# Performance work log

Measured on AMD Instinct MI355X. Metric: run time of the kernel, lower is better.

Reference implementation:

```python
import jax, jax.numpy as jnp
import numpy as np

B, L, D_IN = 32, 200, 64
H = 64          # hidden_size
A = 36          # attention_size
NEG_SLOPE = 0.01  # torch LeakyReLU default


def setup_inputs() -> dict:
    key = jax.random.key(0)
    ks = jax.random.split(key, 7)
    s_ln = 1.0 / np.sqrt(D_IN)
    s_w1 = 1.0 / np.sqrt(3 * H)
    s_w2 = 1.0 / np.sqrt(A)
    return {
        "x": jax.random.normal(ks[0], (B, L, D_IN), dtype=jnp.float32),
        "ln_w": jax.random.uniform(ks[1], (D_IN, H), minval=-s_ln, maxval=s_ln, dtype=jnp.float32),
        "ln_b": jax.random.uniform(ks[2], (H,), minval=-s_ln, maxval=s_ln, dtype=jnp.float32),
        "w1": jax.random.uniform(ks[3], (3 * H, A), minval=-s_w1, maxval=s_w1, dtype=jnp.float32),
        "b1": jax.random.uniform(ks[4], (A,), minval=-s_w1, maxval=s_w1, dtype=jnp.float32),
        "w2": jax.random.uniform(ks[5], (A,), minval=-s_w2, maxval=s_w2, dtype=jnp.float32),
        "b2": jax.random.uniform(ks[6], (), minval=-s_w2, maxval=s_w2, dtype=jnp.float32),
    }


def reference(x, ln_w, ln_b, w1, b1, w2, b2):
    # x: [B, L, D_in] -> h: [B, L, H]
    h = jnp.einsum("bld,dh->blh", x, ln_w) + ln_b
    Ld = h.shape[1]
    Hd = h.shape[-1]
    # The torch code concatenates (x1, x2, x1*x2) where x1[b,i,j]=h[b,j],
    # x2[b,i,j]=h[b,i]. Split w1 accordingly instead of materializing the
    # [B,L,L,3H] concat tensor.
    w1a, w1b, w1c = w1[:Hd], w1[Hd:2 * Hd], w1[2 * Hd:]
    a = jnp.einsum("bjh,ha->bja", h, w1a)          # x1 contribution (depends on j)
    c = jnp.einsum("bih,ha->bia", h, w1b)          # x2 contribution (depends on i)
    cross = jnp.einsum("bih,bjh,ha->bija", h, h, w1c)  # (x1*x2) contribution
    pre = a[:, None, :, :] + c[:, :, None, :] + cross + b1   # [B,L,L,A]
    act = jax.nn.leaky_relu(pre, negative_slope=NEG_SLOPE)
    score = jnp.einsum("bija,a->bij", act, w2) + b2          # [B,L,L]
    mask = jnp.tril(jnp.ones((Ld, Ld), dtype=score.dtype))   # causal (incl. diag)
    score = score * mask
    return jnp.einsum("bij,bjh->bih", score, h)               # [B,L,H]
```

## Files before the change

kernel.cpp:

```cpp
#include <hip/hip_runtime.h>

#define B 32
#define L 200
#define DIN 64
#define H 64
#define A 36

typedef __attribute__((ext_vector_type(8))) short short8;
typedef __attribute__((ext_vector_type(4))) float floatx4;
typedef __attribute__((ext_vector_type(8))) float floatx8;

static __device__ __forceinline__ short f2bf(float f) {
    union { float f; unsigned u; } v; v.f = f;
    unsigned r = (v.u + 0x7FFF + ((v.u >> 16) & 1)) >> 16;
    return (short)r;
}

__global__ __launch_bounds__(256) void prep_kernel(
    const float* __restrict__ x, const float* __restrict__ ln_w,
    const float* __restrict__ ln_b, const float* __restrict__ w1,
    float* __restrict__ h_out, float* __restrict__ cc_out, short* __restrict__ hb16_out,
    float* __restrict__ w1a_r, float* __restrict__ w1c_r)
{
    int wave = threadIdx.x >> 6;
    int lane = threadIdx.x & 63;
    int bl = __builtin_amdgcn_readfirstlane(blockIdx.x * 4 + wave);
    const float* xr = x + (size_t)bl * DIN;
    float p0 = ln_b[lane], p1 = 0.f;
    #pragma unroll
    for (int d = 0; d < DIN; d += 2) {
        p0 = fmaf(xr[d],     ln_w[d * H + lane],       p0);
        p1 = fmaf(xr[d + 1], ln_w[(d + 1) * H + lane], p1);
    }
    float acc = p0 + p1;
    __shared__ float hrow[4][H];
    hrow[wave][lane] = acc;
    h_out[(size_t)bl * H + lane] = acc;
    int j = bl % L;
    hb16_out[(size_t)bl * H + (lane ^ ((j & 7) << 3))] = f2bf(acc);
    if (lane < A) {
        float s0 = 0.f, s1 = 0.f;
        #pragma unroll
        for (int hh = 0; hh < H; hh += 2) {
            s0 = fmaf(hrow[wave][hh],     w1[(H + hh) * A + lane],     s0);
            s1 = fmaf(hrow[wave][hh + 1], w1[(H + hh + 1) * A + lane], s1);
        }
        cc_out[(size_t)bl * A + lane] = s0 + s1;
    }
    if (blockIdx.x == 0) {
        for (int idx = threadIdx.x; idx < 2 * 3 * 64 * 8; idx += 256) {
            int e = idx & 7, ln = (idx >> 3) & 63, sn = idx >> 9;
            int s = sn / 3, n = sn - 3 * s;
            int k = s * 32 + (ln >> 4) * 8 + e;
            int c = n * 16 + (ln & 15);
            w1a_r[idx] = (c < A) ? w1[k * A + c] : 0.f;
            w1c_r[idx] = (c < A) ? w1[(2 * H + k) * A + c] : 0.f;
        }
    }
}

__global__ __launch_bounds__(256) void score_kernel(
    const float* __restrict__ h, const short* __restrict__ hb16,
    const float* __restrict__ cc, const float* __restrict__ w1a_r,
    const float* __restrict__ w1c_r, const float* __restrict__ b1,
    const float* __restrict__ w2, const float* __restrict__ b2,
    float* __restrict__ out)
{
    int blk = blockIdx.x;
    int b  = blk / 50;
    int g  = 49 - (blk - b * 50);
    int wave = threadIdx.x >> 6;
    int lane = threadIdx.x & 63;
    int i = __builtin_amdgcn_readfirstlane(4 * g + wave);
    int l15 = lane & 15, l4 = lane >> 4;

    __shared__ __align__(16) short tile[208 * 64];

    const short* hb16b = hb16 + (size_t)b * L * H;
    const float* h_b   = h + (size_t)b * L * H;

    int maxrow = 4 * g + 3;
    int nch = (((maxrow | 15) + 1) + 7) >> 3;
    for (int c = wave; c < nch; c += 4) {
        int j = c * 8 + (lane >> 3); if (j > L - 1) j = L - 1;
        const short* src = hb16b + (size_t)j * H + (lane & 7) * 8;
        __builtin_amdgcn_global_load_lds(
            (const __attribute__((address_space(1))) void*)src,
            (__attribute__((address_space(3))) void*)&tile[c * 512],
            16, 0, 0);
    }

    const float* hi = h_b + (size_t)i * H;
    float b2v = b2[0];
    float ccl = (lane < A) ? (cc[((size_t)b * L + i) * A + lane] + b1[lane]) : 0.f;
    float w2l = (lane < A) ? w2[lane] : 0.f;
    float w2v[3][4], cbv[3][4];
    #pragma unroll
    for (int n = 0; n < 3; ++n) {
        #pragma unroll
        for (int r = 0; r < 4; ++r) {
            int a = n * 16 + l4 * 4 + r;
            cbv[n][r] = __shfl(ccl, a, 64);
            w2v[n][r] = __shfl(w2l, a, 64);
        }
    }
    short8 afrag[2][3];
    #pragma unroll
    for (int s = 0; s < 2; ++s) {
        float hik[8];
        #pragma unroll
        for (int e = 0; e < 8; ++e) hik[e] = hi[s * 32 + l4 * 8 + e];
        #pragma unroll
        for (int n = 0; n < 3; ++n) {
            floatx8 wa = *(const floatx8*)&w1a_r[(((s * 3 + n) * 64) + lane) * 8];
            floatx8 wc = *(const floatx8*)&w1c_r[(((s * 3 + n) * 64) + lane) * 8];
            #pragma unroll
            for (int e = 0; e < 8; ++e)
                afrag[s][n][e] = f2bf(fmaf(hik[e], wc[e], wa[e]));
        }
    }
    __syncthreads();

    float oacc[4] = {0.f, 0.f, 0.f, 0.f};
    int mmax = (i >> 4) + 1;
    int sw = (l15 & 7) << 3;

    const short* brow0 = tile + l15 * 64;
    short8 bfc0 = *(const short8*)(brow0 + ((l4 * 8) ^ sw));
    short8 bfc1 = *(const short8*)(brow0 + ((32 + l4 * 8) ^ sw));

    for (int m = 0; m < mmax; ++m) {
        short8 bfn0, bfn1;
        if (m + 1 < mmax) {
            const short* brown = tile + ((m + 1) * 16 + l15) * 64;
            bfn0 = *(const short8*)(brown + ((l4 * 8) ^ sw));
            bfn1 = *(const short8*)(brown + ((32 + l4 * 8) ^ sw));
        }
        int row = m * 16 + l15;
        floatx4 c0 = {cbv[0][0], cbv[0][1], cbv[0][2], cbv[0][3]};
        floatx4 c1 = {cbv[1][0], cbv[1][1], cbv[1][2], cbv[1][3]};
        floatx4 c2 = {cbv[2][0], cbv[2][1], cbv[2][2], cbv[2][3]};
        c0 = __builtin_amdgcn_mfma_f32_16x16x32_bf16(afrag[0][0], bfc0, c0, 0, 0, 0);
        c1 = __builtin_amdgcn_mfma_f32_16x16x32_bf16(afrag[0][1], bfc0, c1, 0, 0, 0);
        c2 = __builtin_amdgcn_mfma_f32_16x16x32_bf16(afrag[0][2], bfc0, c2, 0, 0, 0);
        c0 = __builtin_amdgcn_mfma_f32_16x16x32_bf16(afrag[1][0], bfc1, c0, 0, 0, 0);
        c1 = __builtin_amdgcn_mfma_f32_16x16x32_bf16(afrag[1][1], bfc1, c1, 0, 0, 0);
        c2 = __builtin_amdgcn_mfma_f32_16x16x32_bf16(afrag[1][2], bfc1, c2, 0, 0, 0);
        float sp0 = 0.f, sp1 = 0.f, sp2 = 0.f;
        #pragma unroll
        for (int r = 0; r < 4; ++r) {
            sp0 = fmaf(fmaxf(c0[r], 0.01f * c0[r]), w2v[0][r], sp0);
            sp1 = fmaf(fmaxf(c1[r], 0.01f * c1[r]), w2v[1][r], sp1);
            sp2 = fmaf(fmaxf(c2[r], 0.01f * c2[r]), w2v[2][r], sp2);
        }
        float sp = (sp0 + sp1) + sp2;
        sp += __shfl_xor(sp, 16, 64);
        sp += __shfl_xor(sp, 32, 64);
        float sc = (row <= i) ? sp + b2v : 0.f;

        const float* hjb = h_b + (size_t)(m * 16) * H + lane;
        #pragma unroll
        for (int rb = 0; rb < 4; ++rb) {
            #pragma unroll
            for (int q = 0; q < 4; ++q) {
                int jq = rb * 4 + q;
                float sq = __int_as_float(
                    __builtin_amdgcn_readlane(__float_as_int(sc), jq));
                float hv = hjb[jq * H];
                oacc[rb] = fmaf(sq, hv, oacc[rb]);
            }
        }
        bfc0 = bfn0;
        bfc1 = bfn1;
    }

    out[((size_t)b * L + i) * H + lane] = (oacc[0] + oacc[1]) + (oacc[2] + oacc[3]);
}

extern "C" void kernel_launch(void* const* d_in, const int* in_sizes, int n_in,
                              void* d_out, int out_size, void* d_ws, size_t ws_size,
                              hipStream_t stream) {
    const float* x    = (const float*)d_in[0];
    const float* ln_w = (const float*)d_in[1];
    const float* ln_b = (const float*)d_in[2];
    const float* w1   = (const float*)d_in[3];
    const float* b1   = (const float*)d_in[4];
    const float* w2   = (const float*)d_in[5];
    const float* b2   = (const float*)d_in[6];
    float* out = (float*)d_out;

    float* h_ws   = (float*)d_ws;
    float* cc_ws  = h_ws + (size_t)B * L * H;
    short* hb16_ws = (short*)(cc_ws + (size_t)B * L * A);
    float* w1a_r  = (float*)(hb16_ws + (size_t)B * L * H);
    float* w1c_r  = w1a_r + 3072;

    prep_kernel<<<(B * L) / 4, 256, 0, stream>>>(x, ln_w, ln_b, w1, h_ws, cc_ws,
                                                 hb16_ws, w1a_r, w1c_r);
    score_kernel<<<B * 50, 256, 0, stream>>>(h_ws, hb16_ws, cc_ws, w1a_r, w1c_r,
                                             b1, w2, b2, out);
}
```

Before: 38.28 us.

## Move x2 projection into score kernel and process two j-tiles per iteration

Drops the per-row cc projection (h·w1b) from the prep kernel and recomputes it inside the score kernel from the register-resident h_i values, using a repacked w1b and cross-lane shuffles. This removes the cc workspace write/read and prep's shared-memory pass. The score loop is unrolled to handle two 16-row j tiles per iteration with interleaved MFMAs, replacing the prior register double-buffering of B fragments, and launch_bounds is removed from score_kernel. The cost is more register pressure and extra per-block FMAs in the score kernel.

```diff
diff --git a/kernel.cpp b/kernel.cpp
--- a/kernel.cpp
+++ b/kernel.cpp
@@ -19,8 +19,8 @@
 __global__ __launch_bounds__(256) void prep_kernel(
     const float* __restrict__ x, const float* __restrict__ ln_w,
     const float* __restrict__ ln_b, const float* __restrict__ w1,
-    float* __restrict__ h_out, float* __restrict__ cc_out, short* __restrict__ hb16_out,
-    float* __restrict__ w1a_r, float* __restrict__ w1c_r)
+    float* __restrict__ h_out, short* __restrict__ hb16_out,
+    float* __restrict__ w1a_r, float* __restrict__ w1b_r, float* __restrict__ w1c_r)
 {
     int wave = threadIdx.x >> 6;
     int lane = threadIdx.x & 63;
@@ -33,35 +33,26 @@
         p1 = fmaf(xr[d + 1], ln_w[(d + 1) * H + lane], p1);
     }
     float acc = p0 + p1;
-    __shared__ float hrow[4][H];
-    hrow[wave][lane] = acc;
     h_out[(size_t)bl * H + lane] = acc;
     int j = bl % L;
     hb16_out[(size_t)bl * H + (lane ^ ((j & 7) << 3))] = f2bf(acc);
-    if (lane < A) {
-        float s0 = 0.f, s1 = 0.f;
-        #pragma unroll
-        for (int hh = 0; hh < H; hh += 2) {
-            s0 = fmaf(hrow[wave][hh],     w1[(H + hh) * A + lane],     s0);
-            s1 = fmaf(hrow[wave][hh + 1], w1[(H + hh + 1) * A + lane], s1);
-        }
-        cc_out[(size_t)bl * A + lane] = s0 + s1;
-    }
     if (blockIdx.x == 0) {
         for (int idx = threadIdx.x; idx < 2 * 3 * 64 * 8; idx += 256) {
             int e = idx & 7, ln = (idx >> 3) & 63, sn = idx >> 9;
             int s = sn / 3, n = sn - 3 * s;
             int k = s * 32 + (ln >> 4) * 8 + e;
             int c = n * 16 + (ln & 15);
-            w1a_r[idx] = (c < A) ? w1[k * A + c] : 0.f;
-            w1c_r[idx] = (c < A) ? w1[(2 * H + k) * A + c] : 0.f;
-        }
-    }
-}
-
-__global__ __launch_bounds__(256) void score_kernel(
+            bool cv = c < A;
+            w1a_r[idx] = cv ? w1[k * A + c] : 0.f;
+            w1b_r[idx] = cv ? w1[(H + k) * A + c] : 0.f;
+            w1c_r[idx] = cv ? w1[(2 * H + k) * A + c] : 0.f;
+        }
+    }
+}
+
+__global__ void score_kernel(
     const float* __restrict__ h, const short* __restrict__ hb16,
-    const float* __restrict__ cc, const float* __restrict__ w1a_r,
+    const float* __restrict__ w1a_r, const float* __restrict__ w1b_r,
     const float* __restrict__ w1c_r, const float* __restrict__ b1,
     const float* __restrict__ w2, const float* __restrict__ b2,
     float* __restrict__ out)
@@ -92,31 +83,44 @@
 
     const float* hi = h_b + (size_t)i * H;
     float b2v = b2[0];
-    float ccl = (lane < A) ? (cc[((size_t)b * L + i) * A + lane] + b1[lane]) : 0.f;
-    float w2l = (lane < A) ? w2[lane] : 0.f;
+    float hik[2][8];
+    #pragma unroll
+    for (int s = 0; s < 2; ++s) {
+        floatx8 hv = *(const floatx8*)(hi + s * 32 + l4 * 8);
+        #pragma unroll
+        for (int e = 0; e < 8; ++e) hik[s][e] = hv[e];
+    }
+    float ccn[3];
+    short8 afrag[2][3];
+    #pragma unroll
+    for (int n = 0; n < 3; ++n) ccn[n] = 0.f;
+    #pragma unroll
+    for (int s = 0; s < 2; ++s) {
+        #pragma unroll
+        for (int n = 0; n < 3; ++n) {
+            int base = (((s * 3 + n) * 64) + lane) * 8;
+            floatx8 wa = *(const floatx8*)&w1a_r[base];
+            floatx8 wb = *(const floatx8*)&w1b_r[base];
+            floatx8 wc = *(const floatx8*)&w1c_r[base];
+            #pragma unroll
+            for (int e = 0; e < 8; ++e) {
+                afrag[s][n][e] = f2bf(fmaf(hik[s][e], wc[e], wa[e]));
+                ccn[n] = fmaf(hik[s][e], wb[e], ccn[n]);
+            }
+        }
+    }
     float w2v[3][4], cbv[3][4];
     #pragma unroll
     for (int n = 0; n < 3; ++n) {
+        ccn[n] += __shfl_xor(ccn[n], 16, 64);
+        ccn[n] += __shfl_xor(ccn[n], 32, 64);
+        int c = n * 16 + l15;
+        float cb = (c < A) ? (ccn[n] + b1[c]) : 0.f;
         #pragma unroll
         for (int r = 0; r < 4; ++r) {
             int a = n * 16 + l4 * 4 + r;
-            cbv[n][r] = __shfl(ccl, a, 64);
-            w2v[n][r] = __shfl(w2l, a, 64);
-        }
-    }
-    short8 afrag[2][3];
-    #pragma unroll
-    for (int s = 0; s < 2; ++s) {
-        float hik[8];
-        #pragma unroll
-        for (int e = 0; e < 8; ++e) hik[e] = hi[s * 32 + l4 * 8 + e];
-        #pragma unroll
-        for (int n = 0; n < 3; ++n) {
-            floatx8 wa = *(const floatx8*)&w1a_r[(((s * 3 + n) * 64) + lane) * 8];
-            floatx8 wc = *(const floatx8*)&w1c_r[(((s * 3 + n) * 64) + lane) * 8];
-            #pragma unroll
-            for (int e = 0; e < 8; ++e)
-                afrag[s][n][e] = f2bf(fmaf(hik[e], wc[e], wa[e]));
+            cbv[n][r] = __shfl(cb, l4 * 4 + r, 16);
+            w2v[n][r] = (a < A) ? w2[a] : 0.f;
         }
     }
     __syncthreads();
@@ -124,40 +128,92 @@
     float oacc[4] = {0.f, 0.f, 0.f, 0.f};
     int mmax = (i >> 4) + 1;
     int sw = (l15 & 7) << 3;
-
-    const short* brow0 = tile + l15 * 64;
-    short8 bfc0 = *(const short8*)(brow0 + ((l4 * 8) ^ sw));
-    short8 bfc1 = *(const short8*)(brow0 + ((32 + l4 * 8) ^ sw));
-
-    for (int m = 0; m < mmax; ++m) {
-        short8 bfn0, bfn1;
-        if (m + 1 < mmax) {
-            const short* brown = tile + ((m + 1) * 16 + l15) * 64;
-            bfn0 = *(const short8*)(brown + ((l4 * 8) ^ sw));
-            bfn1 = *(const short8*)(brown + ((32 + l4 * 8) ^ sw));
-        }
+    int m = 0;
+
+    for (; m + 1 < mmax; m += 2) {
+        int rowA = m * 16 + l15, rowB = rowA + 16;
+        const short* browA = tile + rowA * 64;
+        const short* browB = tile + rowB * 64;
+        short8 a0 = *(const short8*)(browA + ((l4 * 8) ^ sw));
+        short8 a1 = *(const short8*)(browA + ((32 + l4 * 8) ^ sw));
+        short8 bb0 = *(const short8*)(browB + ((l4 * 8) ^ sw));
+        short8 bb1 = *(const short8*)(browB + ((32 + l4 * 8) ^ sw));
+        floatx4 cA0 = {cbv[0][0], cbv[0][1], cbv[0][2], cbv[0][3]};
+        floatx4 cA1 = {cbv[1][0], cbv[1][1], cbv[1][2], cbv[1][3]};
+        floatx4 cA2 = {cbv[2][0], cbv[2][1], cbv[2][2], cbv[2][3]};
+        floatx4 cB0 = cA0, cB1 = cA1, cB2 = cA2;
+        cA0 = __builtin_amdgcn_mfma_f32_16x16x32_bf16(afrag[0][0], a0, cA0, 0, 0, 0);
+        cB0 = __builtin_amdgcn_mfma_f32_16x16x32_bf16(afrag[0][0], bb0, cB0, 0, 0, 0);
+        cA1 = __builtin_amdgcn_mfma_f32_16x16x32_bf16(afrag[0][1], a0, cA1, 0, 0, 0);
+        cB1 = __builtin_amdgcn_mfma_f32_16x16x32_bf16(afrag[0][1], bb0, cB1, 0, 0, 0);
+        cA2 = __builtin_amdgcn_mfma_f32_16x16x32_bf16(afrag[0][2], a0, cA2, 0, 0, 0);
+        cB2 = __builtin_amdgcn_mfma_f32_16x16x32_bf16(afrag[0][2], bb0, cB2, 0, 0, 0);
+        cA0 = __builtin_amdgcn_mfma_f32_16x16x32_bf16(afrag[1][0], a1, cA0, 0, 0, 0);
+        cB0 = __builtin_amdgcn_mfma_f32_16x16x32_bf16(afrag[1][0], bb1, cB0, 0, 0, 0);
+        cA1 = __builtin_amdgcn_mfma_f32_16x16x32_bf16(afrag[1][1], a1, cA1, 0, 0, 0);
+        cB1 = __builtin_amdgcn_mfma_f32_16x16x32_bf16(afrag[1][1], bb1, cB1, 0, 0, 0);
+        cA2 = __builtin_amdgcn_mfma_f32_16x16x32_bf16(afrag[1][2], a1, cA2, 0, 0, 0);
+        cB2 = __builtin_amdgcn_mfma_f32_16x16x32_bf16(afrag[1][2], bb1, cB2, 0, 0, 0);
+        float sA0 = 0.f, sA1 = 0.f, sA2 = 0.f, sB0 = 0.f, sB1 = 0.f, sB2 = 0.f;
+        #pragma unroll
+        for (int r = 0; r < 4; ++r) {
+            sA0 = fmaf(fmaxf(cA0[r], 0.01f * cA0[r]), w2v[0][r], sA0);
+            sB0 = fmaf(fmaxf(cB0[r], 0.01f * cB0[r]), w2v[0][r], sB0);
+            sA1 = fmaf(fmaxf(cA1[r], 0.01f * cA1[r]), w2v[1][r], sA1);
+            sB1 = fmaf(fmaxf(cB1[r], 0.01f * cB1[r]), w2v[1][r], sB1);
+            sA2 = fmaf(fmaxf(cA2[r], 0.01f * cA2[r]), w2v[2][r], sA2);
+            sB2 = fmaf(fmaxf(cB2[r], 0.01f * cB2[r]), w2v[2][r], sB2);
+        }
+        float spA = (sA0 + sA1) + sA2;
+        float spB = (sB0 + sB1) + sB2;
+        spA += __shfl_xor(spA, 16, 64);
+        spB += __shfl_xor(spB, 16, 64);
+        spA += __shfl_xor(spA, 32, 64);
+        spB += __shfl_xor(spB, 32, 64);
+        float scA = (rowA <= i) ? spA + b2v : 0.f;
+        float scB = (rowB <= i) ? spB + b2v : 0.f;
+
+        const float* hjA = h_b + (size_t)(m * 16) * H + lane;
+        const float* hjB = hjA + 16 * H;
+        #pragma unroll
+        for (int rb = 0; rb < 4; ++rb) {
+            #pragma unroll
+            for (int q = 0; q < 4; ++q) {
+                int jq = rb * 4 + q;
+                float sqA = __int_as_float(
+                    __builtin_amdgcn_readlane(__float_as_int(scA), jq));
+                float sqB = __int_as_float(
+                    __builtin_amdgcn_readlane(__float_as_int(scB), jq));
+                oacc[rb] = fmaf(sqA, hjA[jq * H], oacc[rb]);
+                oacc[rb] = fmaf(sqB, hjB[jq * H], oacc[rb]);
+            }
+        }
+    }
+    if (m < mmax) {
         int row = m * 16 + l15;
+        const short* brow = tile + row * 64;
+        short8 a0 = *(const short8*)(brow + ((l4 * 8) ^ sw));
+        short8 a1 = *(const short8*)(brow + ((32 + l4 * 8) ^ sw));
         floatx4 c0 = {cbv[0][0], cbv[0][1], cbv[0][2], cbv[0][3]};
         floatx4 c1 = {cbv[1][0], cbv[1][1], cbv[1][2], cbv[1][3]};
         floatx4 c2 = {cbv[2][0], cbv[2][1], cbv[2][2], cbv[2][3]};
-        c0 = __builtin_amdgcn_mfma_f32_16x16x32_bf16(afrag[0][0], bfc0, c0, 0, 0, 0);
-        c1 = __builtin_amdgcn_mfma_f32_16x16x32_bf16(afrag[0][1], bfc0, c1, 0, 0, 0);
-        c2 = __builtin_amdgcn_mfma_f32_16x16x32_bf16(afrag[0][2], bfc0, c2, 0, 0, 0);
-        c0 = __builtin_amdgcn_mfma_f32_16x16x32_bf16(afrag[1][0], bfc1, c0, 0, 0, 0);
-        c1 = __builtin_amdgcn_mfma_f32_16x16x32_bf16(afrag[1][1], bfc1, c1, 0, 0, 0);
-        c2 = __builtin_amdgcn_mfma_f32_16x16x32_bf16(afrag[1][2], bfc1, c2, 0, 0, 0);
-        float sp0 = 0.f, sp1 = 0.f, sp2 = 0.f;
+        c0 = __builtin_amdgcn_mfma_f32_16x16x32_bf16(afrag[0][0], a0, c0, 0, 0, 0);
+        c1 = __builtin_amdgcn_mfma_f32_16x16x32_bf16(afrag[0][1], a0, c1, 0, 0, 0);
+        c2 = __builtin_amdgcn_mfma_f32_16x16x32_bf16(afrag[0][2], a0, c2, 0, 0, 0);
+        c0 = __builtin_amdgcn_mfma_f32_16x16x32_bf16(afrag[1][0], a1, c0, 0, 0, 0);
+        c1 = __builtin_amdgcn_mfma_f32_16x16x32_bf16(afrag[1][1], a1, c1, 0, 0, 0);
+        c2 = __builtin_amdgcn_mfma_f32_16x16x32_bf16(afrag[1][2], a1, c2, 0, 0, 0);
+        float s0 = 0.f, s1 = 0.f, s2 = 0.f;
         #pragma unroll
         for (int r = 0; r < 4; ++r) {
-            sp0 = fmaf(fmaxf(c0[r], 0.01f * c0[r]), w2v[0][r], sp0);
-            sp1 = fmaf(fmaxf(c1[r], 0.01f * c1[r]), w2v[1][r], sp1);
-            sp2 = fmaf(fmaxf(c2[r], 0.01f * c2[r]), w2v[2][r], sp2);
-        }
-        float sp = (sp0 + sp1) + sp2;
+            s0 = fmaf(fmaxf(c0[r], 0.01f * c0[r]), w2v[0][r], s0);
+            s1 = fmaf(fmaxf(c1[r], 0.01f * c1[r]), w2v[1][r], s1);
+            s2 = fmaf(fmaxf(c2[r], 0.01f * c2[r]), w2v[2][r], s2);
+        }
+        float sp = (s0 + s1) + s2;
         sp += __shfl_xor(sp, 16, 64);
         sp += __shfl_xor(sp, 32, 64);
         float sc = (row <= i) ? sp + b2v : 0.f;
-
         const float* hjb = h_b + (size_t)(m * 16) * H + lane;
         #pragma unroll
         for (int rb = 0; rb < 4; ++rb) {
@@ -166,12 +222,9 @@
                 int jq = rb * 4 + q;
                 float sq = __int_as_float(
                     __builtin_amdgcn_readlane(__float_as_int(sc), jq));
-                float hv = hjb[jq * H];
-                oacc[rb] = fmaf(sq, hv, oacc[rb]);
+                oacc[rb] = fmaf(sq, hjb[jq * H], oacc[rb]);
             }
         }
-        bfc0 = bfn0;
-        bfc1 = bfn1;
     }
 
     out[((size_t)b * L + i) * H + lane] = (oacc[0] + oacc[1]) + (oacc[2] + oacc[3]);
@@ -190,13 +243,13 @@
     float* out = (float*)d_out;
 
     float* h_ws   = (float*)d_ws;
-    float* cc_ws  = h_ws + (size_t)B * L * H;
-    short* hb16_ws = (short*)(cc_ws + (size_t)B * L * A);
+    short* hb16_ws = (short*)(h_ws + (size_t)B * L * H);
     float* w1a_r  = (float*)(hb16_ws + (size_t)B * L * H);
-    float* w1c_r  = w1a_r + 3072;
-
-    prep_kernel<<<(B * L) / 4, 256, 0, stream>>>(x, ln_w, ln_b, w1, h_ws, cc_ws,
-                                                 hb16_ws, w1a_r, w1c_r);
-    score_kernel<<<B * 50, 256, 0, stream>>>(h_ws, hb16_ws, cc_ws, w1a_r, w1c_r,
+    float* w1b_r  = w1a_r + 3072;
+    float* w1c_r  = w1b_r + 3072;
+
+    prep_kernel<<<(B * L) / 4, 256, 0, stream>>>(x, ln_w, ln_b, w1, h_ws,
+                                                 hb16_ws, w1a_r, w1b_r, w1c_r);
+    score_kernel<<<B * 50, 256, 0, stream>>>(h_ws, hb16_ws, w1a_r, w1b_r, w1c_r,
                                              b1, w2, b2, out);
 }
```

Result: slower. 47.40 us (+23.8%).
